# Optimization experiments

Hardware: AMD Instinct MI355X
Metric: run time of the kernel (lower is better)

The kernel has to match this reference:

```python
import jax, jax.numpy as jnp
import numpy as np
from jax import lax

DT = 1.0 / 120.0
B, T = 4096, 128
TWO_PI = 2.0 * np.pi


def setup_inputs() -> dict:
    key = jax.random.key(0)
    k1, k2, k3, k4 = jax.random.split(key, 4)
    return {
        "params": jax.random.normal(k1, (4,), jnp.float32),
        "covariance_params": jax.random.normal(k2, (7,), jnp.float32),
        "init_states": jax.random.normal(k3, (B, 6), jnp.float32),
        "measurements": jax.random.normal(k4, (B, T, 3), jnp.float32),
    }


def _wrap(a):
    # wrap angle innovation to [-pi, pi]
    return a - TWO_PI * jnp.round(a / TWO_PI)


def _smooth_loss(params, covariance_params, init_state, z):
    # z: [T, 3] measurements of (x, y, theta)
    friction = (jnp.tanh(params[0]) + 1.0) * 0.01
    damping = (jnp.tanh(params[1]) + 1.0) * 0.01
    cp = jax.nn.sigmoid(covariance_params)
    R = jnp.diag(cp[:3])                                    # [3,3] meas noise
    Q = jnp.diag(cp[jnp.array([3, 3, 4, 4, 5, 6])])         # [6,6] proc noise
    I6 = jnp.eye(6, dtype=z.dtype)
    Hm = jnp.zeros((3, 6), z.dtype).at[0, 0].set(1.).at[1, 1].set(1.).at[2, 4].set(1.)
    P0 = 0.01 * I6

    def f_and_F(s):
        # free-sliding puck dynamics: [x, y, dx, dy, th, dth]
        x, y, dx, dy, th, dth = s
        ndx = dx - DT * (damping * dx + friction * jnp.tanh(100. * dx))
        ndy = dy - DT * (damping * dy + friction * jnp.tanh(100. * dy))
        ndth = dth * (1.0 - DT * damping)
        ns = jnp.stack([x + DT * dx, y + DT * dy, ndx, ndy, th + DT * dth, ndth])
        gx = 1.0 - DT * (damping + friction * 100. * (1. - jnp.tanh(100. * dx) ** 2))
        gy = 1.0 - DT * (damping + friction * 100. * (1. - jnp.tanh(100. * dy) ** 2))
        F = (I6.at[0, 2].set(DT).at[1, 3].set(DT).at[4, 5].set(DT)
               .at[2, 2].set(gx).at[3, 3].set(gy).at[5, 5].set(1.0 - DT * damping))
        return ns, F

    def ekf_step(carry, zt):
        s, P = carry
        sp, F = f_and_F(s)
        Pp = F @ P @ F.T + Q
        S = Hm @ Pp @ Hm.T + R
        innov = zt - Hm @ sp
        innov = innov.at[2].set(_wrap(innov[2]))
        K = jnp.linalg.solve(S, Hm @ Pp).T          # Pp H^T S^-1
        s_new = sp + K @ innov
        P_new = (I6 - K @ Hm) @ Pp
        return (s_new, P_new), (s_new, P_new, sp, Pp, F)

    _, (sf, Pf, sp, Pp, Fs) = lax.scan(ekf_step, (init_state, P0), z)

    # RTS backward pass
    def rts_step(carry, inp):
        s_next, P_next = carry
        s_f, P_f, sp_n, Pp_n, F_n = inp
        G = jnp.linalg.solve(Pp_n, F_n @ P_f).T     # P_f F^T Pp^{-1}
        s_s = s_f + G @ (s_next - sp_n)
        P_s = P_f + G @ (P_next - Pp_n) @ G.T
        return (s_s, P_s), (s_s, P_s)

    inp = (sf[:-1], Pf[:-1], sp[1:], Pp[1:], Fs[1:])
    _, (s_sm_head, P_sm_head) = lax.scan(rts_step, (sf[-1], Pf[-1]), inp, reverse=True)
    s_sm = jnp.concatenate([s_sm_head, sf[-1:]], 0)   # [T,6]
    P_sm = jnp.concatenate([P_sm_head, Pf[-1:]], 0)   # [T,6,6]

    # log-lik style loss vs measurements[2:] (as in compute_loss)
    zz, st, Pt = z[2:], s_sm[2:], P_sm[2:]
    Sv = jnp.einsum('ij,tjk,lk->til', Hm, Pt, Hm) + R  # [T-2,3,3] meas-space var
    innov_xy = zz[:, :2] - st[:, :2]
    a = zz[:, 2] - st[:, 4]
    a = jnp.where(a > 1.5 * np.pi, a - TWO_PI, a)
    a = jnp.where(a < -1.5 * np.pi, a + TWO_PI, a)
    innov = jnp.concatenate([innov_xy, a[:, None]], 1)
    sign, logdet = jnp.linalg.slogdet(Sv)
    return jnp.sum(sign * jnp.exp(logdet) + jnp.einsum('ti,tij,tj->t', innov, Sv, innov))


def reference(params, covariance_params, init_states, measurements):
    per_seg = jax.vmap(_smooth_loss, in_axes=(None, None, 0, 0))(
        params, covariance_params, init_states, measurements)
    return jnp.sum(per_seg)
```

## Files before the change

kernel.cpp:

```cpp
#include <hip/hip_runtime.h>
#include <cmath>


namespace {

constexpr int B = 4096;
constexpr int T = 128;
constexpr int NT = B * 3;
constexpr int CPB = 64;
constexpr int NBLK = NT / CPB;
constexpr int RBLK = 512;
constexpr int RTH = 256;

constexpr float DTc     = 1.0f / 120.0f;
constexpr float TWO_PIc = 6.28318530717958647692f;
constexpr float PI_1_5  = 4.71238898038468985769f;
constexpr float INV_2PI = 0.15915494309189533577f;

__device__ __forceinline__ float frcp(float x) { return __builtin_amdgcn_rcpf(x); }

__device__ __forceinline__ float fast_tanh(float x) {
  float e = __expf(2.0f * x);
  return 1.0f - 2.0f * frcp(e + 1.0f);
}
__device__ __forceinline__ float sigmoidf(float x) {
  return frcp(1.0f + __expf(-x));
}

__global__ __launch_bounds__(256) void ztrans_kernel(
    const float* __restrict__ z, float* __restrict__ zt,
    float* __restrict__ out) {
  __shared__ float tile[96 * 65];
  const int tid = threadIdx.x;
  if (blockIdx.x == 0 && tid == 0) out[0] = 0.0f;
  const int bs = blockIdx.x & 63;
  const int bt = blockIdx.x >> 6;
  const int s0 = bs * 64, t0 = bt * 32;

  const float* __restrict__ zbase = z + (size_t)s0 * 384 + t0 * 3;
#pragma unroll
  for (int k = 0; k < 6; k++) {
    const int idx = tid + k * 256;
    const int sl = idx / 24;
    const int c4 = idx - sl * 24;
    const float4 v4 = *(const float4*)(zbase + (size_t)sl * 384 + c4 * 4);
    tile[(c4 * 4 + 0) * 65 + sl] = v4.x;
    tile[(c4 * 4 + 1) * 65 + sl] = v4.y;
    tile[(c4 * 4 + 2) * 65 + sl] = v4.z;
    tile[(c4 * 4 + 3) * 65 + sl] = v4.w;
  }
  __syncthreads();
#pragma unroll
  for (int k = 0; k < 24; k++) {
    const int idx = tid + k * 256;
    const int r  = idx >> 6;
    const int sl = idx & 63;
    const int fc = r >> 5;
    const int tl = r & 31;
    zt[((size_t)fc * T + t0 + tl) * B + s0 + sl] = tile[(tl * 3 + fc) * 65 + sl];
  }
}

__global__ __launch_bounds__(CPB, 1) void filt_kernel(
    const float* __restrict__ params, const float* __restrict__ covp,
    const float* __restrict__ init_states, const float* __restrict__ zt,
    float2* __restrict__ aq) {
  const int lane = threadIdx.x;
  const int blk  = blockIdx.x;
  const int f    = blk >> 6;
  const int seq  = ((blk & 63) << 6) + lane;

  __shared__ float4 h4s[127 * CPB];
  __shared__ float  p11s[T * CPB];

  const float friction = (fast_tanh(params[0]) + 1.0f) * 0.01f;
  const float damping  = (fast_tanh(params[1]) + 1.0f) * 0.01f;
  float cp[7];
#pragma unroll
  for (int i = 0; i < 7; i++) cp[i] = sigmoidf(covp[i]);
  const float dcoef = 1.0f - DTc * damping;
  const bool isTH = (f == 2);
  const float q0 = isTH ? cp[5] : cp[3];
  const float q1 = isTH ? cp[6] : cp[4];
  const float r  = cp[f];

  const int pidx = (f == 0) ? 0 : (f == 1) ? 1 : 4;
  const int vidx = (f == 0) ? 2 : (f == 1) ? 3 : 5;
  float p = init_states[seq * 6 + pidx];
  float v = init_states[seq * 6 + vidx];
  float P00 = 0.01f, P01 = 0.0f, P11 = 0.01f;

  const float* __restrict__ ztf = zt + (size_t)f * T * B + seq;

  float zr[8];
#pragma unroll
  for (int k = 0; k < 8; k++) zr[k] = ztf[(size_t)k * B];
  float zlast = 0.0f;

#define FWD_BODY(t, REFILL)                                                  \
  {                                                                          \
    const float zc = zr[(t) & 7];                                            \
    if (REFILL) zr[(t) & 7] = ztf[(size_t)((t) + 8) * B];                    \
    float g, tv;                                                             \
    if (!isTH) {                                                             \
      const float th = fast_tanh(100.0f * v);                                \
      tv = v - DTc * (damping * v + friction * th);                          \
      g = 1.0f - DTc * (damping + 100.0f * friction * (1.0f - th * th));     \
    } else {                                                                 \
      tv = dcoef * v;                                                        \
      g = dcoef;                                                             \
    }                                                                        \
    const float tp = p + DTc * v;                                            \
    const float u = P01 + DTc * P11;                                         \
    const float Pp00 = P00 + DTc * P01 + DTc * u + q0;                       \
    const float Pp01 = g * u;                                                \
    const float Pp11 = g * (g * P11) + q1;                                   \
    const float iS = frcp(Pp00 + r);                                         \
    const float K0 = Pp00 * iS;                                              \
    const float K1 = Pp01 * iS;                                              \
    float e = zc - tp;                                                       \
    if (isTH) e = e - TWO_PIc * rintf(e * INV_2PI);                          \
    p = tp + K0 * e;                                                         \
    v = tv + K1 * e;                                                         \
    const float om = 1.0f - K0;                                              \
    P00 = om * Pp00;                                                         \
    P01 = om * Pp01;                                                         \
    P11 = Pp11 - K1 * Pp01;                                                  \
    if ((t) < 127) h4s[(t) * CPB + lane] = make_float4(p, v, P00, P01);      \
    p11s[(t) * CPB + lane] = P11;                                            \
    if ((t) == 127) zlast = zc;                                              \
  }

#pragma unroll 8
  for (int t = 0; t < 120; t++) FWD_BODY(t, true)
#pragma unroll
  for (int t = 120; t < 128; t++) FWD_BODY(t, false)
#undef FWD_BODY

  {
    float e = zlast - p;
    if (isTH) {
      if (e >  PI_1_5) e -= TWO_PIc;
      if (e < -PI_1_5) e += TWO_PIc;
    }
    const float a = P00 + r;
    aq[((size_t)f * T + (T - 1)) * B + seq] = make_float2(a, a * e * e);
  }

  float sp_ = p, sv_ = v, Ps00 = P00, Ps01 = P01, Ps11 = P11;

  float4 h4r[4];
  float  p11r[4];
  float  zrb[8];
#pragma unroll
  for (int k = 0; k < 4; k++) {
    h4r[k]  = h4s[(126 - k) * CPB + lane];
    p11r[k] = p11s[(126 - k) * CPB + lane];
  }
#pragma unroll
  for (int k = 0; k < 8; k++) zrb[k] = ztf[(size_t)(126 - k) * B];

#define BWD_BODY(i, RH4, RZ)                                                 \
  {                                                                          \
    const int n = 126 - (i);                                                 \
    const float4 h4 = h4r[(i) & 3];                                          \
    const float f11 = p11r[(i) & 3];                                         \
    const float zn_ = zrb[(i) & 7];                                          \
    if (RH4) {                                                               \
      h4r[(i) & 3]  = h4s[(n - 4) * CPB + lane];                             \
      p11r[(i) & 3] = p11s[(n - 4) * CPB + lane];                            \
    }                                                                        \
    if (RZ) zrb[(i) & 7] = ztf[(size_t)(n - 8) * B];                         \
    const float fp = h4.x, fv = h4.y, f00 = h4.z, f01 = h4.w;                \
    float g, tv;                                                             \
    if (!isTH) {                                                             \
      const float th = fast_tanh(100.0f * fv);                               \
      tv = fv - DTc * (damping * fv + friction * th);                        \
      g = 1.0f - DTc * (damping + 100.0f * friction * (1.0f - th * th));     \
    } else {                                                                 \
      tv = dcoef * fv;                                                       \
      g = dcoef;                                                             \
    }                                                                        \
    const float tp = fp + DTc * fv;                                          \
    const float u = f01 + DTc * f11;                                         \
    const float Pp00 = f00 + DTc * f01 + DTc * u + q0;                       \
    const float Pp01 = g * u;                                                \
    const float Pp11 = g * (g * f11) + q1;                                   \
    const float idet = frcp(Pp00 * Pp11 - Pp01 * Pp01);                      \
    const float W00 = f00, W01 = DTc * f00 + g * f01;                        \
    const float W10 = f01, W11 = DTc * f01 + g * f11;                        \
    const float G00 = (W00 * Pp11 - W01 * Pp01) * idet;                      \
    const float G01 = (W01 * Pp00 - W00 * Pp01) * idet;                      \
    const float G10 = (W10 * Pp11 - W11 * Pp01) * idet;                      \
    const float G11 = (W11 * Pp00 - W10 * Pp01) * idet;                      \
    const float ds0 = sp_ - tp, ds1 = sv_ - tv;                              \
    const float np = fp + G00 * ds0 + G01 * ds1;                             \
    const float nv = fv + G10 * ds0 + G11 * ds1;                             \
    const float M00 = Ps00 - Pp00, M01 = Ps01 - Pp01, M11 = Ps11 - Pp11;     \
    const float GM00 = G00 * M00 + G01 * M01, GM01 = G00 * M01 + G01 * M11;  \
    const float GM10 = G10 * M00 + G11 * M01, GM11 = G10 * M01 + G11 * M11;  \
    Ps00 = f00 + GM00 * G00 + GM01 * G01;                                    \
    Ps01 = f01 + GM00 * G10 + GM01 * G11;                                    \
    Ps11 = f11 + GM10 * G10 + GM11 * G11;                                    \
    sp_ = np;                                                                \
    sv_ = nv;                                                                \
    const float a = Ps00 + r;                                                \
    float e = zn_ - np;                                                      \
    if (isTH) {                                                              \
      if (e >  PI_1_5) e -= TWO_PIc;                                         \
      if (e < -PI_1_5) e += TWO_PIc;                                         \
    }                                                                        \
    aq[((size_t)f * T + n) * B + seq] = make_float2(a, a * e * e);           \
  }

#pragma unroll 8
  for (int i = 0; i < 112; i++) BWD_BODY(i, true, true)
#pragma unroll
  for (int i = 112; i < 125; i++)
    BWD_BODY(i, (126 - i) >= 6, (126 - i) >= 10)
#undef BWD_BODY
}

__global__ __launch_bounds__(RTH) void reduce_kernel(
    const float4* __restrict__ aq4, float* __restrict__ out) {
  const int tid = threadIdx.x;
  constexpr int HB = B / 2;
  constexpr int NTERM4 = 126 * HB;
  float part = 0.0f;
  for (int idx = blockIdx.x * RTH + tid; idx < NTERM4; idx += RTH * RBLK) {
    const int t = 2 + (idx >> 11);
    const int s4 = idx & (HB - 1);
    const float4 a0 = aq4[((size_t)0 * T + t) * HB + s4];
    const float4 a1 = aq4[((size_t)1 * T + t) * HB + s4];
    const float4 a2 = aq4[((size_t)2 * T + t) * HB + s4];
    part += a0.x * a1.x * a2.x + (a0.y + a1.y + a2.y);
    part += a0.z * a1.z * a2.z + (a0.w + a1.w + a2.w);
  }
#pragma unroll
  for (int off = 32; off > 0; off >>= 1) part += __shfl_down(part, off);
  __shared__ float red[RTH / 64];
  if ((tid & 63) == 0) red[tid >> 6] = part;
  __syncthreads();
  if (tid == 0) {
    float s = 0.0f;
#pragma unroll
    for (int w = 0; w < RTH / 64; w++) s += red[w];
    atomicAdd(out, s);
  }
}

}

extern "C" void kernel_launch(void* const* d_in, const int* in_sizes, int n_in,
                              void* d_out, int out_size, void* d_ws, size_t ws_size,
                              hipStream_t stream) {
  const float* params      = (const float*)d_in[0];
  const float* covp        = (const float*)d_in[1];
  const float* init_states = (const float*)d_in[2];
  const float* z           = (const float*)d_in[3];
  float* out = (float*)d_out;

  const size_t ztB = (size_t)T * NT * sizeof(float);
  const size_t aqB = (size_t)T * NT * sizeof(float2);
  const size_t needBytes = ztB + aqB;

  if (ws_size >= needBytes) {
    float*  ztp = (float*)d_ws;
    float2* aqp = (float2*)((char*)d_ws + ztB);
    ztrans_kernel<<<256, 256, 0, stream>>>(z, ztp, out);
    filt_kernel<<<NBLK, CPB, 0, stream>>>(params, covp, init_states, ztp, aqp);
    reduce_kernel<<<RBLK, RTH, 0, stream>>>((const float4*)aqp, out);
  } else {
    hipMemsetAsync(d_out, 0, sizeof(float), stream);
  }
}
```

Before: 122.4 us.

## Pair RTS smoother steps into affine composition and reduce quadratic terms in-kernel

The backward RTS smoother now handles two timesteps per iteration. It builds both gains independently, then composes them into a single affine map, so the serial dependency chain on the smoothed state and covariance is roughly halved. The quadratic innovation term is summed per thread and wave-reduced with an atomic inside the filter kernel, so only the variance term is written to memory. The reduce kernel reads half the data and uses fewer blocks. In exchange each step does more arithmetic and register pressure rises, and regrouping the smoother arithmetic can change floating-point rounding.

```diff
diff --git a/kernel.cpp b/kernel.cpp
--- a/kernel.cpp
+++ b/kernel.cpp
@@ -9,7 +9,7 @@
 constexpr int NT = B * 3;
 constexpr int CPB = 64;
 constexpr int NBLK = NT / CPB;
-constexpr int RBLK = 512;
+constexpr int RBLK = 256;
 constexpr int RTH = 256;
 
 constexpr float DTc     = 1.0f / 120.0f;
@@ -64,7 +64,7 @@
 __global__ __launch_bounds__(CPB, 1) void filt_kernel(
     const float* __restrict__ params, const float* __restrict__ covp,
     const float* __restrict__ init_states, const float* __restrict__ zt,
-    float2* __restrict__ aq) {
+    float* __restrict__ av, float* __restrict__ out) {
   const int lane = threadIdx.x;
   const int blk  = blockIdx.x;
   const int f    = blk >> 6;
@@ -137,6 +137,8 @@
   for (int t = 120; t < 128; t++) FWD_BODY(t, false)
 #undef FWD_BODY
 
+  float qsum = 0.0f;
+
   {
     float e = zlast - p;
     if (isTH) {
@@ -144,7 +146,8 @@
       if (e < -PI_1_5) e += TWO_PIc;
     }
     const float a = P00 + r;
-    aq[((size_t)f * T + (T - 1)) * B + seq] = make_float2(a, a * e * e);
+    av[((size_t)f * T + (T - 1)) * B + seq] = a;
+    qsum += a * e * e;
   }
 
   float sp_ = p, sv_ = v, Ps00 = P00, Ps01 = P01, Ps11 = P11;
@@ -160,81 +163,159 @@
 #pragma unroll
   for (int k = 0; k < 8; k++) zrb[k] = ztf[(size_t)(126 - k) * B];
 
-#define BWD_BODY(i, RH4, RZ)                                                 \
+#define BUILD_G(H4, F11, G00,G01,G10,G11, TP,TV, PP00,PP01,PP11)             \
+    float G00, G01, G10, G11, TP, TV, PP00, PP01, PP11;                      \
+    {                                                                        \
+      const float fp_ = (H4).x, fv_ = (H4).y, f00_ = (H4).z, f01_ = (H4).w;  \
+      float g_;                                                              \
+      if (!isTH) {                                                           \
+        const float th_ = fast_tanh(100.0f * fv_);                           \
+        TV = fv_ - DTc * (damping * fv_ + friction * th_);                   \
+        g_ = 1.0f - DTc * (damping + 100.0f * friction * (1.0f - th_ * th_));\
+      } else {                                                               \
+        TV = dcoef * fv_;                                                    \
+        g_ = dcoef;                                                          \
+      }                                                                      \
+      TP = fp_ + DTc * fv_;                                                  \
+      const float u_ = f01_ + DTc * (F11);                                   \
+      PP00 = f00_ + DTc * f01_ + DTc * u_ + q0;                              \
+      PP01 = g_ * u_;                                                        \
+      PP11 = g_ * (g_ * (F11)) + q1;                                         \
+      const float idet_ = frcp(PP00 * PP11 - PP01 * PP01);                   \
+      const float W01_ = DTc * f00_ + g_ * f01_;                             \
+      const float W11_ = DTc * f01_ + g_ * (F11);                            \
+      G00 = (f00_ * PP11 - W01_ * PP01) * idet_;                             \
+      G01 = (W01_ * PP00 - f00_ * PP01) * idet_;                             \
+      G10 = (f01_ * PP11 - W11_ * PP01) * idet_;                             \
+      G11 = (W11_ * PP00 - f01_ * PP01) * idet_;                             \
+    }
+
+#define CONG3(G00,G01,G10,G11, P00_,P01_,P11_, O00,O01,O11)                  \
+    {                                                                        \
+      const float t0_ = (G00)*(P00_) + (G01)*(P01_);                         \
+      const float t1_ = (G00)*(P01_) + (G01)*(P11_);                         \
+      const float t2_ = (G10)*(P00_) + (G11)*(P01_);                         \
+      const float t3_ = (G10)*(P01_) + (G11)*(P11_);                         \
+      O00 = t0_*(G00) + t1_*(G01);                                           \
+      O01 = t0_*(G10) + t1_*(G11);                                           \
+      O11 = t2_*(G10) + t3_*(G11);                                           \
+    }
+
+#define PAIR_BODY(I0, RH4A, RH4B, RZA, RZB)                                  \
   {                                                                          \
-    const int n = 126 - (i);                                                 \
-    const float4 h4 = h4r[(i) & 3];                                          \
-    const float f11 = p11r[(i) & 3];                                         \
-    const float zn_ = zrb[(i) & 7];                                          \
-    if (RH4) {                                                               \
-      h4r[(i) & 3]  = h4s[(n - 4) * CPB + lane];                             \
-      p11r[(i) & 3] = p11s[(n - 4) * CPB + lane];                            \
+    const int iA = (I0), iB = (I0) + 1;                                      \
+    const int nA = 126 - iA, nB = 126 - iB;                                  \
+    const float4 h4a = h4r[iA & 3]; const float f11a = p11r[iA & 3];         \
+    const float4 h4b = h4r[iB & 3]; const float f11b = p11r[iB & 3];         \
+    const float za = zrb[iA & 7], zb = zrb[iB & 7];                          \
+    if (RH4A) { h4r[iA & 3]  = h4s[(nA - 4) * CPB + lane];                   \
+                p11r[iA & 3] = p11s[(nA - 4) * CPB + lane]; }                \
+    if (RH4B) { h4r[iB & 3]  = h4s[(nB - 4) * CPB + lane];                   \
+                p11r[iB & 3] = p11s[(nB - 4) * CPB + lane]; }                \
+    if (RZA) zrb[iA & 7] = ztf[(size_t)(nA - 8) * B];                        \
+    if (RZB) zrb[iB & 7] = ztf[(size_t)(nB - 8) * B];                        \
+    BUILD_G(h4a, f11a, Ga00,Ga01,Ga10,Ga11, tpa,tva, Ppa00,Ppa01,Ppa11)      \
+    BUILD_G(h4b, f11b, Gb00,Gb01,Gb10,Gb11, tpb,tvb, Ppb00,Ppb01,Ppb11)      \
+    const float Aa0 = h4a.x - (Ga00*tpa + Ga01*tva);                         \
+    const float Aa1 = h4a.y - (Ga10*tpa + Ga11*tva);                         \
+    const float Ab0 = h4b.x - (Gb00*tpb + Gb01*tvb);                         \
+    const float Ab1 = h4b.y - (Gb10*tpb + Gb11*tvb);                         \
+    const float H00 = Gb00*Ga00 + Gb01*Ga10;                                 \
+    const float H01 = Gb00*Ga01 + Gb01*Ga11;                                 \
+    const float H10 = Gb10*Ga00 + Gb11*Ga10;                                 \
+    const float H11 = Gb10*Ga01 + Gb11*Ga11;                                 \
+    const float Bs0 = Ab0 + Gb00*Aa0 + Gb01*Aa1;                             \
+    const float Bs1 = Ab1 + Gb10*Aa0 + Gb11*Aa1;                             \
+    float Oa00, Oa01, Oa11, Ob00, Ob01, Ob11, Oc00, Oc01, Oc11;              \
+    CONG3(Ga00,Ga01,Ga10,Ga11, Ppa00,Ppa01,Ppa11, Oa00,Oa01,Oa11)            \
+    const float Ca00 = h4a.z - Oa00, Ca01 = h4a.w - Oa01;                    \
+    const float Ca11 = f11a - Oa11;                                          \
+    CONG3(Gb00,Gb01,Gb10,Gb11, Ppb00,Ppb01,Ppb11, Ob00,Ob01,Ob11)            \
+    const float Cb00 = h4b.z - Ob00, Cb01 = h4b.w - Ob01;                    \
+    const float Cb11 = f11b - Ob11;                                          \
+    CONG3(Gb00,Gb01,Gb10,Gb11, Ca00,Ca01,Ca11, Oc00,Oc01,Oc11)               \
+    const float C200 = Cb00 + Oc00, C201 = Cb01 + Oc01, C211 = Cb11 + Oc11;  \
+                                   \
+    const float np = Aa0 + Ga00*sp_ + Ga01*sv_;                              \
+    const float t0a = Ga00*Ps00 + Ga01*Ps01;                                 \
+    const float t1a = Ga00*Ps01 + Ga01*Ps11;                                 \
+    const float Pn00 = Ca00 + t0a*Ga00 + t1a*Ga01;                           \
+    float Ph00, Ph01, Ph11;                                                  \
+    CONG3(H00,H01,H10,H11, Ps00,Ps01,Ps11, Ph00,Ph01,Ph11)                   \
+    const float sm0 = Bs0 + H00*sp_ + H01*sv_;                               \
+    const float sm1 = Bs1 + H10*sp_ + H11*sv_;                               \
+    Ps00 = C200 + Ph00; Ps01 = C201 + Ph01; Ps11 = C211 + Ph11;              \
+    sp_ = sm0; sv_ = sm1;                                                    \
+    float eA = za - np;                                                      \
+    const float aA = Pn00 + r;                                               \
+    if (isTH) {                                                              \
+      if (eA >  PI_1_5) eA -= TWO_PIc;                                       \
+      if (eA < -PI_1_5) eA += TWO_PIc;                                       \
     }                                                                        \
-    if (RZ) zrb[(i) & 7] = ztf[(size_t)(n - 8) * B];                         \
-    const float fp = h4.x, fv = h4.y, f00 = h4.z, f01 = h4.w;                \
-    float g, tv;                                                             \
-    if (!isTH) {                                                             \
-      const float th = fast_tanh(100.0f * fv);                               \
-      tv = fv - DTc * (damping * fv + friction * th);                        \
-      g = 1.0f - DTc * (damping + 100.0f * friction * (1.0f - th * th));     \
-    } else {                                                                 \
-      tv = dcoef * fv;                                                       \
-      g = dcoef;                                                             \
+    av[((size_t)f * T + nA) * B + seq] = aA;                                 \
+    qsum += aA * eA * eA;                                                    \
+    float eB = zb - sp_;                                                     \
+    const float aB = Ps00 + r;                                               \
+    if (isTH) {                                                              \
+      if (eB >  PI_1_5) eB -= TWO_PIc;                                       \
+      if (eB < -PI_1_5) eB += TWO_PIc;                                       \
     }                                                                        \
-    const float tp = fp + DTc * fv;                                          \
-    const float u = f01 + DTc * f11;                                         \
-    const float Pp00 = f00 + DTc * f01 + DTc * u + q0;                       \
-    const float Pp01 = g * u;                                                \
-    const float Pp11 = g * (g * f11) + q1;                                   \
-    const float idet = frcp(Pp00 * Pp11 - Pp01 * Pp01);                      \
-    const float W00 = f00, W01 = DTc * f00 + g * f01;                        \
-    const float W10 = f01, W11 = DTc * f01 + g * f11;                        \
-    const float G00 = (W00 * Pp11 - W01 * Pp01) * idet;                      \
-    const float G01 = (W01 * Pp00 - W00 * Pp01) * idet;                      \
-    const float G10 = (W10 * Pp11 - W11 * Pp01) * idet;                      \
-    const float G11 = (W11 * Pp00 - W10 * Pp01) * idet;                      \
-    const float ds0 = sp_ - tp, ds1 = sv_ - tv;                              \
-    const float np = fp + G00 * ds0 + G01 * ds1;                             \
-    const float nv = fv + G10 * ds0 + G11 * ds1;                             \
-    const float M00 = Ps00 - Pp00, M01 = Ps01 - Pp01, M11 = Ps11 - Pp11;     \
-    const float GM00 = G00 * M00 + G01 * M01, GM01 = G00 * M01 + G01 * M11;  \
-    const float GM10 = G10 * M00 + G11 * M01, GM11 = G10 * M01 + G11 * M11;  \
-    Ps00 = f00 + GM00 * G00 + GM01 * G01;                                    \
-    Ps01 = f01 + GM00 * G10 + GM01 * G11;                                    \
-    Ps11 = f11 + GM10 * G10 + GM11 * G11;                                    \
-    sp_ = np;                                                                \
-    sv_ = nv;                                                                \
-    const float a = Ps00 + r;                                                \
-    float e = zn_ - np;                                                      \
-    if (isTH) {                                                              \
-      if (e >  PI_1_5) e -= TWO_PIc;                                         \
-      if (e < -PI_1_5) e += TWO_PIc;                                         \
-    }                                                                        \
-    aq[((size_t)f * T + n) * B + seq] = make_float2(a, a * e * e);           \
-  }
-
-#pragma unroll 8
-  for (int i = 0; i < 112; i++) BWD_BODY(i, true, true)
-#pragma unroll
-  for (int i = 112; i < 125; i++)
-    BWD_BODY(i, (126 - i) >= 6, (126 - i) >= 10)
-#undef BWD_BODY
+    av[((size_t)f * T + nB) * B + seq] = aB;                                 \
+    qsum += aB * eB * eB;                                                    \
+  }
+
+#pragma unroll 4
+  for (int j = 0; j < 56; j++) PAIR_BODY(2 * j, true, true, true, true)
+#pragma unroll
+  for (int j = 56; j < 62; j++)
+    PAIR_BODY(2 * j, (122 - 2 * j) >= 0, (121 - 2 * j) >= 0,
+              (118 - 2 * j) >= 0, (117 - 2 * j) >= 0)
+
+  {
+    const float4 h4a = h4r[124 & 3];
+    const float f11a = p11r[124 & 3];
+    const float za = zrb[124 & 7];
+    BUILD_G(h4a, f11a, Ga00,Ga01,Ga10,Ga11, tpa,tva, Ppa00,Ppa01,Ppa11)
+    const float Aa0 = h4a.x - (Ga00*tpa + Ga01*tva);
+    const float np = Aa0 + Ga00*sp_ + Ga01*sv_;
+    const float u0 = Ga00*Ppa00 + Ga01*Ppa01;
+    const float u1 = Ga00*Ppa01 + Ga01*Ppa11;
+    const float Ca00 = h4a.z - (u0*Ga00 + u1*Ga01);
+    const float t0a = Ga00*Ps00 + Ga01*Ps01;
+    const float t1a = Ga00*Ps01 + Ga01*Ps11;
+    const float Pn00 = Ca00 + t0a*Ga00 + t1a*Ga01;
+    float eA = za - np;
+    const float aA = Pn00 + r;
+    if (isTH) {
+      if (eA >  PI_1_5) eA -= TWO_PIc;
+      if (eA < -PI_1_5) eA += TWO_PIc;
+    }
+    av[((size_t)f * T + 2) * B + seq] = aA;
+    qsum += aA * eA * eA;
+  }
+#undef PAIR_BODY
+#undef CONG3
+#undef BUILD_G
+
+#pragma unroll
+  for (int off = 32; off > 0; off >>= 1) qsum += __shfl_down(qsum, off);
+  if (lane == 0) atomicAdd(out, qsum);
 }
 
 __global__ __launch_bounds__(RTH) void reduce_kernel(
-    const float4* __restrict__ aq4, float* __restrict__ out) {
+    const float4* __restrict__ av4, float* __restrict__ out) {
   const int tid = threadIdx.x;
-  constexpr int HB = B / 2;
-  constexpr int NTERM4 = 126 * HB;
+  constexpr int QB = B / 4;
+  constexpr int NTERM4 = 126 * QB;
   float part = 0.0f;
   for (int idx = blockIdx.x * RTH + tid; idx < NTERM4; idx += RTH * RBLK) {
-    const int t = 2 + (idx >> 11);
-    const int s4 = idx & (HB - 1);
-    const float4 a0 = aq4[((size_t)0 * T + t) * HB + s4];
-    const float4 a1 = aq4[((size_t)1 * T + t) * HB + s4];
-    const float4 a2 = aq4[((size_t)2 * T + t) * HB + s4];
-    part += a0.x * a1.x * a2.x + (a0.y + a1.y + a2.y);
-    part += a0.z * a1.z * a2.z + (a0.w + a1.w + a2.w);
+    const int t = 2 + (idx >> 10);
+    const int s4 = idx & (QB - 1);
+    const float4 a0 = av4[((size_t)0 * T + t) * QB + s4];
+    const float4 a1 = av4[((size_t)1 * T + t) * QB + s4];
+    const float4 a2 = av4[((size_t)2 * T + t) * QB + s4];
+    part += a0.x * a1.x * a2.x + a0.y * a1.y * a2.y;
+    part += a0.z * a1.z * a2.z + a0.w * a1.w * a2.w;
   }
 #pragma unroll
   for (int off = 32; off > 0; off >>= 1) part += __shfl_down(part, off);
@@ -261,15 +342,16 @@
   float* out = (float*)d_out;
 
   const size_t ztB = (size_t)T * NT * sizeof(float);
-  const size_t aqB = (size_t)T * NT * sizeof(float2);
-  const size_t needBytes = ztB + aqB;
+  const size_t avB = (size_t)T * NT * sizeof(float);
+  const size_t needBytes = ztB + avB;
 
   if (ws_size >= needBytes) {
-    float*  ztp = (float*)d_ws;
-    float2* aqp = (float2*)((char*)d_ws + ztB);
+    float* ztp = (float*)d_ws;
+    float* avp = (float*)((char*)d_ws + ztB);
     ztrans_kernel<<<256, 256, 0, stream>>>(z, ztp, out);
-    filt_kernel<<<NBLK, CPB, 0, stream>>>(params, covp, init_states, ztp, aqp);
-    reduce_kernel<<<RBLK, RTH, 0, stream>>>((const float4*)aqp, out);
+    filt_kernel<<<NBLK, CPB, 0, stream>>>(params, covp, init_states, ztp,
+                                          avp, out);
+    reduce_kernel<<<RBLK, RTH, 0, stream>>>((const float4*)avp, out);
   } else {
     hipMemsetAsync(d_out, 0, sizeof(float), stream);
   }
```

After: 124.4 us. Within noise of the previous version (+1.6%).
